# Performance work log

Hardware: AMD Instinct MI355X
Metric: run time of the kernel (lower is better)

Reference implementation:

```python
import jax, jax.numpy as jnp
import numpy as np

NUM_LAYERS = 12
D = 256          # d_model
H = 8            # n_head
DK = D // H      # qk_dim = v_dim = 32
FFD = 1024       # ffd_dim
B, L = 32, 448
EPS = 1e-6
MAXLEN = 500


def _sinusoidal_pos_emb(maxlen, hidden_dim):
    depth = hidden_dim / 2
    positions = np.arange(maxlen, dtype=np.float32)[:, None]
    depths = np.arange(depth, dtype=np.float32)[None, :] / depth
    angle_rads = positions * (1.0 / np.power(10000.0, depths))
    pe = np.concatenate([np.sin(angle_rads), np.cos(angle_rads)], axis=-1)
    return jnp.asarray(pe, jnp.float32)


def setup_inputs() -> dict:
    key = jax.random.key(0)
    ks = jax.random.split(key, 16)
    s = 0.02
    inp = {
        "x": jax.random.normal(ks[0], (B, L, D), jnp.float32),
        "mask": jnp.zeros((B, L), jnp.bool_),
        "pos_emb": _sinusoidal_pos_emb(MAXLEN - 1, D)[:L],  # [L, D]
        "Wq": jax.random.normal(ks[1], (NUM_LAYERS, D, D), jnp.float32) * s,
        "bq": jnp.zeros((NUM_LAYERS, D), jnp.float32),
        "Wk": jax.random.normal(ks[2], (NUM_LAYERS, D, D), jnp.float32) * s,
        "bk": jnp.zeros((NUM_LAYERS, D), jnp.float32),
        "Wv": jax.random.normal(ks[3], (NUM_LAYERS, D, D), jnp.float32) * s,
        "bv": jnp.zeros((NUM_LAYERS, D), jnp.float32),
        "Wo": jax.random.normal(ks[4], (NUM_LAYERS, D, D), jnp.float32) * s,
        "bo": jnp.zeros((NUM_LAYERS, D), jnp.float32),
        "W1": jax.random.normal(ks[5], (NUM_LAYERS, D, FFD), jnp.float32) * s,
        "bf1": jnp.zeros((NUM_LAYERS, FFD), jnp.float32),
        "W2": jax.random.normal(ks[6], (NUM_LAYERS, FFD, D), jnp.float32) * s,
        "bf2": jnp.zeros((NUM_LAYERS, D), jnp.float32),
        "ln1_g": jnp.ones((NUM_LAYERS, D), jnp.float32),
        "ln1_b": jnp.zeros((NUM_LAYERS, D), jnp.float32),
        "ln2_g": jnp.ones((NUM_LAYERS, D), jnp.float32),
        "ln2_b": jnp.zeros((NUM_LAYERS, D), jnp.float32),
    }
    return inp


def _layer_norm(x, g, b):
    mu = jnp.mean(x, axis=-1, keepdims=True)
    var = jnp.mean(jnp.square(x - mu), axis=-1, keepdims=True)
    return (x - mu) * jax.lax.rsqrt(var + EPS) * g + b


def _encoder_forward(x, mask, pos_emb, Wq, bq, Wk, bk, Wv, bv, Wo, bo,
                     W1, bf1, W2, bf2, ln1_g, ln1_b, ln2_g, ln2_b):
    Bx, Lx, _ = x.shape
    scale = 1.0 / np.sqrt(DK)
    x = x + pos_emb[None, :Lx, :]
    mask_b = mask[:, None, None, :]  # [B,1,1,L], True = masked
    for i in range(NUM_LAYERS):
        # --- pre-norm attention ---
        nx = _layer_norm(x, ln1_g[i], ln1_b[i])
        q = (nx @ Wq[i] + bq[i]).reshape(Bx, Lx, H, DK)
        k = (nx @ Wk[i] + bk[i]).reshape(Bx, Lx, H, DK)
        v = (nx @ Wv[i] + bv[i]).reshape(Bx, Lx, H, DK)
        dot = jnp.einsum("bihd,bjhd->bhij", q, k) * scale
        dot = jnp.where(mask_b, -10000.0, dot)
        attn = jax.nn.softmax(dot, axis=-1)
        o = jnp.einsum("bhij,bjhd->bihd", attn, v).reshape(Bx, Lx, D)
        x = x + (o @ Wo[i] + bo[i])
        # --- pre-norm FFN (exact GELU, as torch nn.GELU) ---
        nx2 = _layer_norm(x, ln2_g[i], ln2_b[i])
        h = jax.nn.gelu(nx2 @ W1[i] + bf1[i], approximate=False)
        x = x + (h @ W2[i] + bf2[i])
    return x


def reference(x, mask, pos_emb, Wq, bq, Wk, bk, Wv, bv, Wo, bo,
              W1, bf1, W2, bf2, ln1_g, ln1_b, ln2_g, ln2_b):
    return _encoder_forward(x, mask, pos_emb, Wq, bq, Wk, bk, Wv, bv, Wo, bo,
                            W1, bf1, W2, bf2, ln1_g, ln1_b, ln2_g, ln2_b)
```

## Files before the change

kernel.cpp:

```cpp
#include <hip/hip_runtime.h>

#define NL 12
#define DM 256
#define FFDIM 1024
#define BBATCH 32
#define LSEQ 448
#define MTOK (BBATCH*LSEQ)
#define EPSF 1e-6f

typedef __attribute__((ext_vector_type(8))) short bf16x8;
typedef __attribute__((ext_vector_type(4))) float f32x4;
typedef unsigned short u16;
typedef unsigned int u32;

__device__ __forceinline__ u16 f2bf(float f) {
    union { float f; u32 u; } v; v.f = f;
    u32 r = v.u + 0x7fffu + ((v.u >> 16) & 1u);
    return (u16)(r >> 16);
}
__device__ __forceinline__ float gelu_exact(float x) {
    return 0.5f * x * (1.0f + erff(x * 0.70710678118654752f));
}

__global__ __launch_bounds__(256) void add_pos_k(
    const float* __restrict__ x, const float* __restrict__ pe, float* __restrict__ out)
{
    int i = blockIdx.x * 256 + threadIdx.x;
    float4 xv = ((const float4*)x)[i];
    float4 pv = ((const float4*)pe)[i % (LSEQ * DM / 4)];
    float4 r;
    r.x = xv.x + pv.x; r.y = xv.y + pv.y; r.z = xv.z + pv.z; r.w = xv.w + pv.w;
    ((float4*)out)[i] = r;
}

__global__ __launch_bounds__(256) void ln_k(
    const float* __restrict__ x, const float* __restrict__ g,
    const float* __restrict__ b, u16* __restrict__ out)
{
    const int w = threadIdx.x >> 6, lane = threadIdx.x & 63;
    const int row = blockIdx.x * 4 + w;
    float4 v = ((const float4*)(x + (size_t)row * DM))[lane];
    float s = v.x + v.y + v.z + v.w;
#pragma unroll
    for (int off = 32; off; off >>= 1) s += __shfl_xor(s, off);
    float mu = s * (1.0f / 256.0f);
    float d0 = v.x - mu, d1 = v.y - mu, d2 = v.z - mu, d3 = v.w - mu;
    float sq = d0*d0 + d1*d1 + d2*d2 + d3*d3;
#pragma unroll
    for (int off = 32; off; off >>= 1) sq += __shfl_xor(sq, off);
    float rs = rsqrtf(sq * (1.0f / 256.0f) + EPSF);
    float4 gv = ((const float4*)g)[lane];
    float4 bv = ((const float4*)b)[lane];
    ushort4 o;
    o.x = f2bf(d0 * rs * gv.x + bv.x);
    o.y = f2bf(d1 * rs * gv.y + bv.y);
    o.z = f2bf(d2 * rs * gv.z + bv.z);
    o.w = f2bf(d3 * rs * gv.w + bv.w);
    *(ushort4*)(out + (size_t)row * DM + lane * 4) = o;
}

__global__ __launch_bounds__(256) void twt_k(
    const float* __restrict__ in, u16* __restrict__ out,
    int K, int N, int in_lstride, int out_lstride)
{
    __shared__ float tl[32][33];
    const int l = blockIdx.z;
    const int n0 = blockIdx.x * 32, k0 = blockIdx.y * 32;
    const int tx = threadIdx.x & 31, ty = threadIdx.x >> 5;
    const float* src = in + (size_t)l * in_lstride;
#pragma unroll
    for (int i = 0; i < 4; ++i)
        tl[ty + 8*i][tx] = src[(size_t)(k0 + ty + 8*i) * N + n0 + tx];
    __syncthreads();
    u16* dst = out + (size_t)l * out_lstride;
#pragma unroll
    for (int i = 0; i < 4; ++i)
        dst[(size_t)(n0 + ty + 8*i) * K + k0 + tx] = f2bf(tl[tx][ty + 8*i]);
}

__global__ __launch_bounds__(256) void pack_bias_k(
    const float* __restrict__ bq, const float* __restrict__ bk,
    const float* __restrict__ bv, float* __restrict__ bqkv)
{
    int i = blockIdx.x * 256 + threadIdx.x;
    if (i >= NL * 768) return;
    int l = i / 768, c = i % 768;
    float v = (c < 256) ? bq[l*256 + c] : (c < 512) ? bk[l*256 + c - 256] : bv[l*256 + c - 512];
    bqkv[i] = v;
}

__global__ __launch_bounds__(256) void vt_k(
    const u16* __restrict__ qkv, u16* __restrict__ vtg)
{
    __shared__ u16 tl[32][33];
    const int kt = blockIdx.x, h = blockIdx.y, b = blockIdx.z;
    const int tx = threadIdx.x & 31, ty = threadIdx.x >> 5;
#pragma unroll
    for (int i = 0; i < 4; ++i)
        tl[ty + 8*i][tx] = qkv[(size_t)(b*LSEQ + kt*32 + ty + 8*i) * 768 + 512 + h*32 + tx];
    __syncthreads();
#pragma unroll
    for (int i = 0; i < 4; ++i)
        vtg[((size_t)(b*8 + h)*32 + ty + 8*i) * 448 + kt*32 + tx] = tl[tx][ty + 8*i];
}

template<int BN, int EPI>
__global__ __launch_bounds__(256, 2) void mm_k(
    const u16* __restrict__ A, int lda, const u16* __restrict__ Bt,
    const float* __restrict__ bias, void* __restrict__ C, int ldc, int K)
{
    __shared__ u16 As[128 * 32];
    __shared__ u16 Bs[BN * 32];
    constexpr int MT = (BN == 128) ? 4 : 2;
    const int tid = threadIdx.x;
    const int bx = blockIdx.x, by = blockIdx.y;
    const int w = tid >> 6, lane = tid & 63;
    const int lm = lane & 15, lk = lane >> 4;
    const int wm = (BN == 128) ? (w >> 1) : w;
    const int wn = (BN == 128) ? (w & 1) : 0;
    const int m0 = wm * MT * 16;
    const int n0 = wn * 64;
    const int ar = tid >> 2, akg = tid & 3;

    const u16* Ab = A + (size_t)(by * 128) * lda;
    const u16* Bb = Bt + (size_t)(bx * BN) * K;

    f32x4 zz = {0.f, 0.f, 0.f, 0.f};
    f32x4 acc[MT][4];
#pragma unroll
    for (int i = 0; i < MT; ++i)
#pragma unroll
        for (int j = 0; j < 4; ++j) acc[i][j] = zz;

    for (int k0 = 0; k0 < K; k0 += 32) {
        uint4 a0 = *(const uint4*)(Ab + (size_t)ar * lda + k0 + akg*8);
        uint4 a1 = *(const uint4*)(Ab + (size_t)(64 + ar) * lda + k0 + akg*8);
        uint4 b0 = *(const uint4*)(Bb + (size_t)ar * K + k0 + akg*8);
        uint4 b1 = {};
        if constexpr (BN == 128)
            b1 = *(const uint4*)(Bb + (size_t)(64 + ar) * K + k0 + akg*8);
        __syncthreads();
        *(uint4*)&As[ar*32 + akg*8] = a0;
        *(uint4*)&As[(64 + ar)*32 + akg*8] = a1;
        *(uint4*)&Bs[ar*32 + akg*8] = b0;
        if constexpr (BN == 128)
            *(uint4*)&Bs[(64 + ar)*32 + akg*8] = b1;
        __syncthreads();
        bf16x8 af[MT], bfr[4];
#pragma unroll
        for (int mt = 0; mt < MT; ++mt)
            af[mt] = *(const bf16x8*)&As[(m0 + mt*16 + lm)*32 + lk*8];
#pragma unroll
        for (int nt = 0; nt < 4; ++nt)
            bfr[nt] = *(const bf16x8*)&Bs[(n0 + nt*16 + lm)*32 + lk*8];
#pragma unroll
        for (int mt = 0; mt < MT; ++mt)
#pragma unroll
            for (int nt = 0; nt < 4; ++nt)
                acc[mt][nt] = __builtin_amdgcn_mfma_f32_16x16x32_bf16(af[mt], bfr[nt], acc[mt][nt], 0, 0, 0);
    }

    float bv[4];
#pragma unroll
    for (int nt = 0; nt < 4; ++nt) bv[nt] = bias[bx*BN + n0 + nt*16 + lm];
#pragma unroll
    for (int mt = 0; mt < MT; ++mt) {
#pragma unroll
        for (int r = 0; r < 4; ++r) {
            int grow = by*128 + m0 + mt*16 + lk*4 + r;
#pragma unroll
            for (int nt = 0; nt < 4; ++nt) {
                int gcol = bx*BN + n0 + nt*16 + lm;
                float vv = acc[mt][nt][r] + bv[nt];
                if constexpr (EPI == 0) {
                    ((u16*)C)[(size_t)grow * ldc + gcol] = f2bf(vv);
                } else if constexpr (EPI == 1) {
                    ((u16*)C)[(size_t)grow * ldc + gcol] = f2bf(gelu_exact(vv));
                } else {
                    float* p = (float*)C + (size_t)grow * ldc + gcol;
                    *p += vv;
                }
            }
        }
    }
}

__global__ __launch_bounds__(256, 2) void attn_k(
    const u16* __restrict__ qkv, const u16* __restrict__ vtg,
    const unsigned char* __restrict__ mask, u16* __restrict__ ob)
{
    __shared__ u16 Klds[448 * 32];
    __shared__ u16 Plds[4][16 * 64];
    const int tid = threadIdx.x, w = tid >> 6, lane = tid & 63;
    const int lm = lane & 15, lk = lane >> 4;
    const int bid = blockIdx.x;
    const int b = bid >> 4, h = (bid >> 1) & 7, half = bid & 1;
    const size_t rowbase = (size_t)b * LSEQ;

    for (int cid = tid; cid < 448 * 4; cid += 256) {
        int row = cid >> 2, kg = cid & 3;
        *(uint4*)&Klds[row*32 + kg*8] =
            *(const uint4*)(qkv + (rowbase + row)*768 + 256 + h*32 + kg*8);
    }
    unsigned mbits = 0;
#pragma unroll
    for (int t = 0; t < 28; ++t)
        mbits |= (mask[b*LSEQ + t*16 + lm] ? 1u : 0u) << t;
    __syncthreads();

    const u16* Vb = vtg + (size_t)(b*8 + h) * 32 * 448;
    const float scale = 0.17677669529663687f;
    f32x4 zz = {0.f, 0.f, 0.f, 0.f};

    for (int s = w; s < 14; s += 4) {
        const int q0 = half * 224 + s * 16;
        bf16x8 qf = *(const bf16x8*)(qkv + (rowbase + q0 + lm)*768 + h*32 + lk*8);
        f32x4 sc[28];
#pragma unroll
        for (int t = 0; t < 28; ++t) {
            bf16x8 kf = *(const bf16x8*)&Klds[(t*16 + lm)*32 + lk*8];
            sc[t] = __builtin_amdgcn_mfma_f32_16x16x32_bf16(qf, kf, zz, 0, 0, 0);
        }
        float mx[4] = {-1e30f, -1e30f, -1e30f, -1e30f};
#pragma unroll
        for (int t = 0; t < 28; ++t) {
            bool m = (mbits >> t) & 1;
#pragma unroll
            for (int r = 0; r < 4; ++r) {
                float v = m ? -10000.0f : sc[t][r] * scale;
                sc[t][r] = v;
                mx[r] = fmaxf(mx[r], v);
            }
        }
#pragma unroll
        for (int off = 1; off < 16; off <<= 1)
#pragma unroll
            for (int r = 0; r < 4; ++r) mx[r] = fmaxf(mx[r], __shfl_xor(mx[r], off));
        float sum[4] = {0.f, 0.f, 0.f, 0.f};
#pragma unroll
        for (int t = 0; t < 28; ++t)
#pragma unroll
            for (int r = 0; r < 4; ++r) {
                float e = __expf(sc[t][r] - mx[r]);
                sc[t][r] = e;
                sum[r] += e;
            }
#pragma unroll
        for (int off = 1; off < 16; off <<= 1)
#pragma unroll
            for (int r = 0; r < 4; ++r) sum[r] += __shfl_xor(sum[r], off);
        float inv[4];
#pragma unroll
        for (int r = 0; r < 4; ++r) inv[r] = 1.0f / sum[r];

        f32x4 oacc[2] = {zz, zz};
        u16* P = &Plds[w][0];
#pragma unroll
        for (int cc = 0; cc < 7; ++cc) {
#pragma unroll
            for (int tt = 0; tt < 4; ++tt) {
                int t = cc*4 + tt;
#pragma unroll
                for (int r = 0; r < 4; ++r)
                    P[(lk*4 + r)*64 + tt*16 + lm] = f2bf(sc[t][r] * inv[r]);
            }
            bf16x8 pa0 = *(const bf16x8*)&P[lm*64 + lk*8];
            bf16x8 pa1 = *(const bf16x8*)&P[lm*64 + 32 + lk*8];
#pragma unroll
            for (int dt = 0; dt < 2; ++dt) {
                bf16x8 vb0 = *(const bf16x8*)(Vb + (size_t)(dt*16 + lm)*448 + cc*64 + lk*8);
                bf16x8 vb1 = *(const bf16x8*)(Vb + (size_t)(dt*16 + lm)*448 + cc*64 + 32 + lk*8);
                oacc[dt] = __builtin_amdgcn_mfma_f32_16x16x32_bf16(pa0, vb0, oacc[dt], 0, 0, 0);
                oacc[dt] = __builtin_amdgcn_mfma_f32_16x16x32_bf16(pa1, vb1, oacc[dt], 0, 0, 0);
            }
        }
#pragma unroll
        for (int dt = 0; dt < 2; ++dt)
#pragma unroll
            for (int r = 0; r < 4; ++r)
                ob[(rowbase + q0 + lk*4 + r)*256 + h*32 + dt*16 + lm] = f2bf(oacc[dt][r]);
    }
}

extern "C" void kernel_launch(void* const* d_in, const int* in_sizes, int n_in,
                              void* d_out, int out_size, void* d_ws, size_t ws_size,
                              hipStream_t stream)
{
    const float* x_in = (const float*)d_in[0];
    const unsigned char* mask = (const unsigned char*)d_in[1];
    const float* pe   = (const float*)d_in[2];
    const float* Wq = (const float*)d_in[3];
    const float* bq = (const float*)d_in[4];
    const float* Wk = (const float*)d_in[5];
    const float* bk = (const float*)d_in[6];
    const float* Wv = (const float*)d_in[7];
    const float* bv = (const float*)d_in[8];
    const float* Wo = (const float*)d_in[9];
    const float* bo = (const float*)d_in[10];
    const float* W1 = (const float*)d_in[11];
    const float* bf1 = (const float*)d_in[12];
    const float* W2 = (const float*)d_in[13];
    const float* bf2 = (const float*)d_in[14];
    const float* ln1_g = (const float*)d_in[15];
    const float* ln1_b = (const float*)d_in[16];
    const float* ln2_g = (const float*)d_in[17];
    const float* ln2_b = (const float*)d_in[18];

    float* x = (float*)d_out;
    u16* ws = (u16*)d_ws;
    u16* nx   = ws;
    u16* qkv  = nx + 3670016;
    u16* ob   = qkv + 11010048;
    u16* vtg  = ob + 3670016;
    u16* hb   = qkv;
    u16* wqkvt = vtg + 3670016;
    u16* wot  = wqkvt + 2359296;
    u16* w1t  = wot + 786432;
    u16* w2t  = w1t + 3145728;
    float* bqkv = (float*)(w2t + 3145728);

    add_pos_k<<<MTOK * DM / 1024, 256, 0, stream>>>(x_in, pe, x);

    twt_k<<<dim3(8, 8, NL), 256, 0, stream>>>(Wq, wqkvt,          256, 256, 65536, 196608);
    twt_k<<<dim3(8, 8, NL), 256, 0, stream>>>(Wk, wqkvt + 65536,  256, 256, 65536, 196608);
    twt_k<<<dim3(8, 8, NL), 256, 0, stream>>>(Wv, wqkvt + 131072, 256, 256, 65536, 196608);
    twt_k<<<dim3(8, 8, NL), 256, 0, stream>>>(Wo, wot, 256, 256, 65536, 65536);
    twt_k<<<dim3(32, 8, NL), 256, 0, stream>>>(W1, w1t, 256, 1024, 262144, 262144);
    twt_k<<<dim3(8, 32, NL), 256, 0, stream>>>(W2, w2t, 1024, 256, 262144, 262144);
    pack_bias_k<<<(NL * 768 + 255) / 256, 256, 0, stream>>>(bq, bk, bv, bqkv);

    for (int l = 0; l < NL; ++l) {
        ln_k<<<MTOK / 4, 256, 0, stream>>>(x, ln1_g + l*256, ln1_b + l*256, nx);
        mm_k<128, 0><<<dim3(6, 112), 256, 0, stream>>>(
            nx, 256, wqkvt + (size_t)l*196608, bqkv + l*768, qkv, 768, 256);
        vt_k<<<dim3(14, 8, 32), 256, 0, stream>>>(qkv, vtg);
        attn_k<<<512, 256, 0, stream>>>(qkv, vtg, mask, ob);
        mm_k<64, 2><<<dim3(4, 112), 256, 0, stream>>>(
            ob, 256, wot + (size_t)l*65536, bo + l*256, x, 256, 256);
        ln_k<<<MTOK / 4, 256, 0, stream>>>(x, ln2_g + l*256, ln2_b + l*256, nx);
        mm_k<128, 1><<<dim3(8, 112), 256, 0, stream>>>(
            nx, 256, w1t + (size_t)l*262144, bf1 + l*1024, hb, 1024, 256);
        mm_k<64, 2><<<dim3(4, 112), 256, 0, stream>>>(
            hb, 1024, w2t + (size_t)l*262144, bf2 + l*256, x, 256, 1024);
    }
}
```

Measured before the change: 1.750 ms.

## Use direct global-to-LDS loads and split attention into more blocks

GEMM tiles and attention K tiles are now loaded with global_load_lds, which writes global data straight into shared memory without passing through registers. The attention kernel launches 1792 blocks, one 16-row query tile per wave, instead of 512 blocks that each loop over query tiles. It also pads the P staging buffer to reduce LDS bank conflicts and applies the softmax 1/sum after the PV product. The aim is to cut register pressure and load latency and to improve occupancy. The cost is that each block reloads K into LDS more often, since K is now fetched 7 times per head instead of twice.

```diff
diff --git a/kernel.cpp b/kernel.cpp
--- a/kernel.cpp
+++ b/kernel.cpp
@@ -20,6 +20,11 @@
 }
 __device__ __forceinline__ float gelu_exact(float x) {
     return 0.5f * x * (1.0f + erff(x * 0.70710678118654752f));
+}
+__device__ __forceinline__ void gload16(const u16* g, u16* l) {
+    __builtin_amdgcn_global_load_lds(
+        (const __attribute__((address_space(1))) u32*)g,
+        (__attribute__((address_space(3))) u32*)l, 16, 0, 0);
 }
 
 __global__ __launch_bounds__(256) void add_pos_k(
@@ -120,7 +125,7 @@
     const int wn = (BN == 128) ? (w & 1) : 0;
     const int m0 = wm * MT * 16;
     const int n0 = wn * 64;
-    const int ar = tid >> 2, akg = tid & 3;
+    const int lrow = lane >> 2, lcol = (lane & 3) * 8;
 
     const u16* Ab = A + (size_t)(by * 128) * lda;
     const u16* Bb = Bt + (size_t)(bx * BN) * K;
@@ -133,19 +138,23 @@
         for (int j = 0; j < 4; ++j) acc[i][j] = zz;
 
     for (int k0 = 0; k0 < K; k0 += 32) {
-        uint4 a0 = *(const uint4*)(Ab + (size_t)ar * lda + k0 + akg*8);
-        uint4 a1 = *(const uint4*)(Ab + (size_t)(64 + ar) * lda + k0 + akg*8);
-        uint4 b0 = *(const uint4*)(Bb + (size_t)ar * K + k0 + akg*8);
-        uint4 b1 = {};
-        if constexpr (BN == 128)
-            b1 = *(const uint4*)(Bb + (size_t)(64 + ar) * K + k0 + akg*8);
         __syncthreads();
-        *(uint4*)&As[ar*32 + akg*8] = a0;
-        *(uint4*)&As[(64 + ar)*32 + akg*8] = a1;
-        *(uint4*)&Bs[ar*32 + akg*8] = b0;
-        if constexpr (BN == 128)
-            *(uint4*)&Bs[(64 + ar)*32 + akg*8] = b1;
+#pragma unroll
+        for (int i = 0; i < 2; ++i) {
+            int seg = w * 2 + i;
+            gload16(Ab + (size_t)(seg * 16 + lrow) * lda + k0 + lcol, &As[seg * 512]);
+        }
+        if constexpr (BN == 128) {
+#pragma unroll
+            for (int i = 0; i < 2; ++i) {
+                int seg = w * 2 + i;
+                gload16(Bb + (size_t)(seg * 16 + lrow) * K + k0 + lcol, &Bs[seg * 512]);
+            }
+        } else {
+            gload16(Bb + (size_t)(w * 16 + lrow) * K + k0 + lcol, &Bs[w * 512]);
+        }
         __syncthreads();
+
         bf16x8 af[MT], bfr[4];
 #pragma unroll
         for (int mt = 0; mt < MT; ++mt)
@@ -190,96 +199,96 @@
     const unsigned char* __restrict__ mask, u16* __restrict__ ob)
 {
     __shared__ u16 Klds[448 * 32];
-    __shared__ u16 Plds[4][16 * 64];
+    __shared__ u16 Plds[4][16 * 68];
     const int tid = threadIdx.x, w = tid >> 6, lane = tid & 63;
     const int lm = lane & 15, lk = lane >> 4;
     const int bid = blockIdx.x;
-    const int b = bid >> 4, h = (bid >> 1) & 7, half = bid & 1;
+    const int bh = bid / 7, sg = bid % 7;
+    const int b = bh >> 3, h = bh & 7;
     const size_t rowbase = (size_t)b * LSEQ;
 
-    for (int cid = tid; cid < 448 * 4; cid += 256) {
-        int row = cid >> 2, kg = cid & 3;
-        *(uint4*)&Klds[row*32 + kg*8] =
-            *(const uint4*)(qkv + (rowbase + row)*768 + 256 + h*32 + kg*8);
+#pragma unroll
+    for (int i = 0; i < 7; ++i) {
+        int seg = w * 7 + i;
+        gload16(qkv + (rowbase + seg * 16 + (lane >> 2)) * 768 + 256 + h * 32 + (lane & 3) * 8,
+                &Klds[seg * 512]);
     }
     unsigned mbits = 0;
 #pragma unroll
     for (int t = 0; t < 28; ++t)
-        mbits |= (mask[b*LSEQ + t*16 + lm] ? 1u : 0u) << t;
+        mbits |= (mask[b * LSEQ + t * 16 + lm] ? 1u : 0u) << t;
     __syncthreads();
 
-    const u16* Vb = vtg + (size_t)(b*8 + h) * 32 * 448;
+    const u16* Vb = vtg + (size_t)bh * 32 * 448;
     const float scale = 0.17677669529663687f;
     f32x4 zz = {0.f, 0.f, 0.f, 0.f};
 
-    for (int s = w; s < 14; s += 4) {
-        const int q0 = half * 224 + s * 16;
-        bf16x8 qf = *(const bf16x8*)(qkv + (rowbase + q0 + lm)*768 + h*32 + lk*8);
-        f32x4 sc[28];
-#pragma unroll
-        for (int t = 0; t < 28; ++t) {
-            bf16x8 kf = *(const bf16x8*)&Klds[(t*16 + lm)*32 + lk*8];
-            sc[t] = __builtin_amdgcn_mfma_f32_16x16x32_bf16(qf, kf, zz, 0, 0, 0);
-        }
-        float mx[4] = {-1e30f, -1e30f, -1e30f, -1e30f};
-#pragma unroll
-        for (int t = 0; t < 28; ++t) {
-            bool m = (mbits >> t) & 1;
-#pragma unroll
-            for (int r = 0; r < 4; ++r) {
-                float v = m ? -10000.0f : sc[t][r] * scale;
-                sc[t][r] = v;
-                mx[r] = fmaxf(mx[r], v);
-            }
-        }
-#pragma unroll
-        for (int off = 1; off < 16; off <<= 1)
-#pragma unroll
-            for (int r = 0; r < 4; ++r) mx[r] = fmaxf(mx[r], __shfl_xor(mx[r], off));
-        float sum[4] = {0.f, 0.f, 0.f, 0.f};
-#pragma unroll
-        for (int t = 0; t < 28; ++t)
-#pragma unroll
-            for (int r = 0; r < 4; ++r) {
-                float e = __expf(sc[t][r] - mx[r]);
-                sc[t][r] = e;
-                sum[r] += e;
-            }
-#pragma unroll
-        for (int off = 1; off < 16; off <<= 1)
-#pragma unroll
-            for (int r = 0; r < 4; ++r) sum[r] += __shfl_xor(sum[r], off);
-        float inv[4];
-#pragma unroll
-        for (int r = 0; r < 4; ++r) inv[r] = 1.0f / sum[r];
-
-        f32x4 oacc[2] = {zz, zz};
-        u16* P = &Plds[w][0];
-#pragma unroll
-        for (int cc = 0; cc < 7; ++cc) {
-#pragma unroll
-            for (int tt = 0; tt < 4; ++tt) {
-                int t = cc*4 + tt;
-#pragma unroll
-                for (int r = 0; r < 4; ++r)
-                    P[(lk*4 + r)*64 + tt*16 + lm] = f2bf(sc[t][r] * inv[r]);
-            }
-            bf16x8 pa0 = *(const bf16x8*)&P[lm*64 + lk*8];
-            bf16x8 pa1 = *(const bf16x8*)&P[lm*64 + 32 + lk*8];
-#pragma unroll
-            for (int dt = 0; dt < 2; ++dt) {
-                bf16x8 vb0 = *(const bf16x8*)(Vb + (size_t)(dt*16 + lm)*448 + cc*64 + lk*8);
-                bf16x8 vb1 = *(const bf16x8*)(Vb + (size_t)(dt*16 + lm)*448 + cc*64 + 32 + lk*8);
-                oacc[dt] = __builtin_amdgcn_mfma_f32_16x16x32_bf16(pa0, vb0, oacc[dt], 0, 0, 0);
-                oacc[dt] = __builtin_amdgcn_mfma_f32_16x16x32_bf16(pa1, vb1, oacc[dt], 0, 0, 0);
-            }
-        }
-#pragma unroll
-        for (int dt = 0; dt < 2; ++dt)
+    const int q0 = (sg * 4 + w) * 16;
+    bf16x8 qf = *(const bf16x8*)(qkv + (rowbase + q0 + lm) * 768 + h * 32 + lk * 8);
+    f32x4 sc[28];
+#pragma unroll
+    for (int t = 0; t < 28; ++t) {
+        bf16x8 kf = *(const bf16x8*)&Klds[(t*16 + lm)*32 + lk*8];
+        sc[t] = __builtin_amdgcn_mfma_f32_16x16x32_bf16(qf, kf, zz, 0, 0, 0);
+    }
+    float mx[4] = {-1e30f, -1e30f, -1e30f, -1e30f};
+#pragma unroll
+    for (int t = 0; t < 28; ++t) {
+        bool m = (mbits >> t) & 1;
+#pragma unroll
+        for (int r = 0; r < 4; ++r) {
+            float v = m ? -10000.0f : sc[t][r] * scale;
+            sc[t][r] = v;
+            mx[r] = fmaxf(mx[r], v);
+        }
+    }
+#pragma unroll
+    for (int off = 1; off < 16; off <<= 1)
+#pragma unroll
+        for (int r = 0; r < 4; ++r) mx[r] = fmaxf(mx[r], __shfl_xor(mx[r], off));
+    float sum[4] = {0.f, 0.f, 0.f, 0.f};
+#pragma unroll
+    for (int t = 0; t < 28; ++t)
+#pragma unroll
+        for (int r = 0; r < 4; ++r) {
+            float e = __expf(sc[t][r] - mx[r]);
+            sc[t][r] = e;
+            sum[r] += e;
+        }
+#pragma unroll
+    for (int off = 1; off < 16; off <<= 1)
+#pragma unroll
+        for (int r = 0; r < 4; ++r) sum[r] += __shfl_xor(sum[r], off);
+    float inv[4];
+#pragma unroll
+    for (int r = 0; r < 4; ++r) inv[r] = 1.0f / sum[r];
+
+    f32x4 oacc[2] = {zz, zz};
+    u16* P = &Plds[w][0];
+#pragma unroll
+    for (int cc = 0; cc < 7; ++cc) {
+#pragma unroll
+        for (int tt = 0; tt < 4; ++tt) {
+            int t = cc*4 + tt;
 #pragma unroll
             for (int r = 0; r < 4; ++r)
-                ob[(rowbase + q0 + lk*4 + r)*256 + h*32 + dt*16 + lm] = f2bf(oacc[dt][r]);
-    }
+                P[(lk*4 + r)*68 + tt*16 + lm] = f2bf(sc[t][r]);
+        }
+        bf16x8 pa0 = *(const bf16x8*)&P[lm*68 + lk*8];
+        bf16x8 pa1 = *(const bf16x8*)&P[lm*68 + 32 + lk*8];
+#pragma unroll
+        for (int dt = 0; dt < 2; ++dt) {
+            bf16x8 vb0 = *(const bf16x8*)(Vb + (size_t)(dt*16 + lm)*448 + cc*64 + lk*8);
+            bf16x8 vb1 = *(const bf16x8*)(Vb + (size_t)(dt*16 + lm)*448 + cc*64 + 32 + lk*8);
+            oacc[dt] = __builtin_amdgcn_mfma_f32_16x16x32_bf16(pa0, vb0, oacc[dt], 0, 0, 0);
+            oacc[dt] = __builtin_amdgcn_mfma_f32_16x16x32_bf16(pa1, vb1, oacc[dt], 0, 0, 0);
+        }
+    }
+#pragma unroll
+    for (int dt = 0; dt < 2; ++dt)
+#pragma unroll
+        for (int r = 0; r < 4; ++r)
+            ob[(rowbase + q0 + lk*4 + r)*256 + h*32 + dt*16 + lm] = f2bf(oacc[dt][r] * inv[r]);
 }
 
 extern "C" void kernel_launch(void* const* d_in, const int* in_sizes, int n_in,
@@ -334,7 +343,7 @@
         mm_k<128, 0><<<dim3(6, 112), 256, 0, stream>>>(
             nx, 256, wqkvt + (size_t)l*196608, bqkv + l*768, qkv, 768, 256);
         vt_k<<<dim3(14, 8, 32), 256, 0, stream>>>(qkv, vtg);
-        attn_k<<<512, 256, 0, stream>>>(qkv, vtg, mask, ob);
+        attn_k<<<1792, 256, 0, stream>>>(qkv, vtg, mask, ob);
         mm_k<64, 2><<<dim3(4, 112), 256, 0, stream>>>(
             ob, 256, wot + (size_t)l*65536, bo + l*256, x, 256, 256);
         ln_k<<<MTOK / 4, 256, 0, stream>>>(x, ln2_g + l*256, ln2_b + l*256, nx);
```

Measured after the change: 1.710 ms. 2.3% less time.
